# Performance work log

Hardware: AMD Instinct MI355X
Metric: run time of the kernel (lower is better)

Reference implementation:

```python
import jax, jax.numpy as jnp
import numpy as np

N_IN = 2_000_000
N_OUT = 250_000
C_IN = 32
C_OUT = 64
K_VOL = 8  # 2x2x2 kernel, stride 2
EPS = 1e-5


def setup_inputs() -> dict:
    key = jax.random.key(0)
    ks = jax.random.split(key, 6)
    return {
        "in_feats": jax.random.normal(ks[0], (N_IN, C_IN), dtype=jnp.float32),
        "offset_id": jax.random.randint(ks[1], (N_IN,), 0, K_VOL, dtype=jnp.int32),
        "out_idx": jax.random.randint(ks[2], (N_IN,), 0, N_OUT, dtype=jnp.int32),
        "weight": jax.random.normal(ks[3], (K_VOL, C_IN, C_OUT), dtype=jnp.float32) * 0.05,
        "gamma": jnp.ones((3, C_OUT), dtype=jnp.float32),
        "beta": jnp.zeros((3, C_OUT), dtype=jnp.float32),
        "context": jax.random.normal(ks[4], (256,), dtype=jnp.float32),
        "ctx_w": jax.random.normal(ks[5], (256, 2 * C_OUT), dtype=jnp.float32) * 0.02,
        "condition": 1,
    }


def reference(in_feats, offset_id, out_idx, weight, gamma, beta, context, ctx_w, condition):
    # --- sparse conv (stride == kernel): gather-GEMM-scatter per kernel tap ---
    out = jnp.zeros((N_OUT, C_OUT), dtype=in_feats.dtype)
    for k in range(K_VOL):  # fixed small loop over kernel taps
        xk = jnp.where((offset_id == k)[:, None], in_feats, 0.0)  # [N_in, C_in]
        contrib = xk @ weight[k]                                  # [N_in, C_out]
        out = out + jax.ops.segment_sum(contrib, out_idx, num_segments=N_OUT)
    # --- conditional BN (PDNorm-style): per-channel stats, condition-selected affine ---
    mean = jnp.mean(out, axis=0)
    var = jnp.var(out, axis=0)
    normed = (out - mean) * jax.lax.rsqrt(var + EPS)
    normed = normed * gamma[condition] + beta[condition]
    # context modulation: scale/shift from context vector
    scale, shift = jnp.split(context @ ctx_w, 2)  # each [C_out]
    normed = normed * (1.0 + scale) + shift
    # --- ReLU ---
    return jax.nn.relu(normed)
```

## Files before the change

### kernel.cpp

```cpp
#include <hip/hip_runtime.h>

#define N_IN 2000000
#define N_OUT 250000
#define C_IN 32
#define C_OUT 64
#define K_VOL 8
#define EPS 1e-5f
#define CAP 32

#define PT_BLOCKS 7813
#define N_SCAN 250112
#define N_SBLK 977

typedef __attribute__((ext_vector_type(8))) short short8;
typedef __attribute__((ext_vector_type(4))) float f32x4;

#define TA_WHL    250368
#define TA_BSUM   266752
#define TA_SMALL  267776
#define TA_CNT    268288
#define TA_TAPB   518400
#define TA_XG     1018400
#define TA_POS    (TA_XG + N_IN * 32)
#define TA_NEED_BYTES ((size_t)(TA_POS + N_IN) * 4)

#define T1_WT     250000
#define T1_SMALL  266384
#define T1_RLIST  266768
#define T1_NEED_BYTES ((size_t)(T1_RLIST + N_OUT * CAP) * 4)

__global__ __launch_bounds__(256) void k_wpack(const float* __restrict__ w,
                                               ushort* __restrict__ whl) {
    int e = blockIdx.x * 256 + threadIdx.x;
    int c = e >> 11, t = (e >> 9) & 3, l = (e >> 3) & 63, kp = e & 7;
    int j = 4 * c + (l >> 4);
    int n = t * 16 + (l & 15);
    float v = w[kp * 2048 + j * 64 + n];
    unsigned bits = __float_as_uint(v);
    float lo = v - __uint_as_float(bits & 0xFFFF0000u);
    whl[e]         = (ushort)(bits >> 16);
    whl[16384 + e] = (ushort)(__float_as_uint(lo) >> 16);
}


__global__ __launch_bounds__(256) void k_rank(const int* __restrict__ out_idx,
                                              int* __restrict__ cnt,
                                              int* __restrict__ pos0) {
    int i = blockIdx.x * 256 + threadIdx.x;
    if (i < N_IN) pos0[i] = atomicAdd(&cnt[out_idx[i]], 1);
}

__global__ __launch_bounds__(256) void k_scan_a(const int* __restrict__ cnt,
                                                int* __restrict__ S,
                                                int* __restrict__ bsum) {
    __shared__ int sh[256];
    int t = threadIdx.x;
    int g = blockIdx.x * 256 + t;
    int v = cnt[g];
    sh[t] = v;
    __syncthreads();
#pragma unroll
    for (int off = 1; off < 256; off <<= 1) {
        int a = (t >= off) ? sh[t - off] : 0;
        __syncthreads();
        sh[t] += a;
        __syncthreads();
    }
    S[g] = sh[t] - v;
    if (t == 255) bsum[blockIdx.x] = sh[255];
}

__global__ __launch_bounds__(1024) void k_scan_b(int* __restrict__ bsum) {
    __shared__ int sh[1024];
    int t = threadIdx.x;
    int v = (t < N_SBLK) ? bsum[t] : 0;
    sh[t] = v;
    __syncthreads();
#pragma unroll
    for (int off = 1; off < 1024; off <<= 1) {
        int a = (t >= off) ? sh[t - off] : 0;
        __syncthreads();
        sh[t] += a;
        __syncthreads();
    }
    bsum[t] = sh[t] - v;
}

__global__ __launch_bounds__(256) void k_scan_c(int* __restrict__ S,
                                                const int* __restrict__ bsum) {
    int g = blockIdx.x * 256 + threadIdx.x;
    S[g] += bsum[blockIdx.x];
}

__global__ __launch_bounds__(256) void k_scat3(const int* __restrict__ out_idx,
                                               const int* __restrict__ offs,
                                               const int* __restrict__ pos0,
                                               const int* __restrict__ S,
                                               const float* __restrict__ xf,
                                               float* __restrict__ xg,
                                               unsigned char* __restrict__ tb) {
    int lane = threadIdx.x & 63;
    int wid = (blockIdx.x * 256 + threadIdx.x) >> 6;
    int g = lane >> 3, e = lane & 7;
    const int STRIDE = PT_BLOCKS * 4 * 8;
    for (int p0 = wid * 8; p0 < N_IN; p0 += STRIDE) {
        int p = p0 + g;
        float4 x = *(const float4*)(xf + (size_t)p * 32 + e * 4);
        int pos = 0;
        if (e == 0) {
            int o = out_idx[p];
            pos = S[o] + pos0[p];
            tb[pos] = (unsigned char)(offs[p] | ((o & 31) << 3));
        }
        pos = __shfl(pos, g * 8, 64);
        *(float4*)(xg + (size_t)pos * 32 + e * 4) = x;
    }
}

__global__ __launch_bounds__(256) void k_gconv6(const float* __restrict__ xg,
                                                const unsigned char* __restrict__ tb,
                                                const int* __restrict__ Sarr,
                                                const ushort* __restrict__ whl,
                                                float* __restrict__ out) {
    __shared__ float vxl[4 * 4640];
    int lane = threadIdx.x & 63;
    int wv = threadIdx.x >> 6;
    int g = blockIdx.x * 4 + wv;
    int base = g * 16;
    if (base >= N_OUT) return;
    float* VX = vxl + wv * 4640;
    short* XT = (short*)VX;

    int s = Sarr[base];
    int e = Sarr[base + 16];
    int slot = lane >> 3, jq = lane & 7;

    int tgt8[8];
#pragma unroll
    for (int m = 0; m < 8; ++m) {
        int bin0 = m * 16 + (lane & 15);
        tgt8[m] = (((base + (bin0 >> 3)) & 31) << 3) | (bin0 & 7);
    }

    f32x4 acc1[8][2];
#pragma unroll
    for (int m = 0; m < 8; ++m)
#pragma unroll
        for (int n = 0; n < 2; ++n)
            acc1[m][n] = (f32x4){0.f, 0.f, 0.f, 0.f};

    auto LOADBLK = [&](int p0, float4* xvv, int* tvv) {
#pragma unroll
        for (int q = 0; q < 4; ++q) {
            int p = p0 + q * 8 + slot;
            int pc = p < e ? p : e - 1;
            xvv[q] = *(const float4*)(xg + (size_t)pc * 32 + jq * 4);
            tvv[q] = tb[pc];
            if (p >= e) xvv[q] = make_float4(0.f, 0.f, 0.f, 0.f);
        }
    };
    auto STAGE = [&](int bb, const float4* xvv, const int* tvv) {
        short* Xh = XT + bb * 3104;
        short* Xl = Xh + 1536;
        unsigned char* TGb = (unsigned char*)(Xh + 3072);
#pragma unroll
        for (int q = 0; q < 4; ++q) {
            int wpos = ((q ^ (jq & 3)) << 3) + slot;
#pragma unroll
            for (int i = 0; i < 4; ++i) {
                float v = (i == 0) ? xvv[q].x : (i == 1) ? xvv[q].y
                         : (i == 2) ? xvv[q].z : xvv[q].w;
                unsigned b = __float_as_uint(v);
                float lo = v - __uint_as_float(b & 0xFFFF0000u);
                int ch = 4 * jq + i;
                Xh[ch * 48 + wpos] = (short)(b >> 16);
                Xl[ch * 48 + wpos] = (short)(__float_as_uint(lo) >> 16);
            }
            if (jq == 0) TGb[q * 8 + slot] = (unsigned char)tvv[q];
        }
    };

    if (e > s) {
        float4 xv[4], xv2[4];
        int tv[4], tv2[4];
        LOADBLK(s, xv, tv);
        STAGE(0, xv, tv);
        int nIt = (e - s + 31) >> 5;
        for (int it = 0; it < nIt; ++it) {
            int cur = it & 1;
            bool more = (it + 1 < nIt);
            if (more) LOADBLK(s + (it + 1) * 32, xv2, tv2);

            asm volatile("s_waitcnt lgkmcnt(0)" ::: "memory");

            const short* Xh = XT + cur * 3104;
            const short* Xl = Xh + 1536;
            const unsigned char* TGb = (const unsigned char*)(Xh + 3072);
            unsigned long long t8 = *(const unsigned long long*)(TGb + 8 * (lane >> 4));
            int tgv[8];
#pragma unroll
            for (int e2 = 0; e2 < 8; ++e2) tgv[e2] = (int)((t8 >> (8 * e2)) & 0xFF);
            short8 bhf[2], blf[2];
#pragma unroll
            for (int n = 0; n < 2; ++n) {
                int ch = n * 16 + (lane & 15);
                int off = ch * 48 + 8 * ((lane >> 4) ^ ((ch >> 2) & 3));
                bhf[n] = *(const short8*)(Xh + off);
                blf[n] = *(const short8*)(Xl + off);
            }
#pragma unroll
            for (int m = 0; m < 8; ++m) {
                short8 ah;
#pragma unroll
                for (int e2 = 0; e2 < 8; ++e2)
                    ah[e2] = (tgv[e2] == tgt8[m]) ? (short)0x3F80 : (short)0;
#pragma unroll
                for (int n = 0; n < 2; ++n) {
                    acc1[m][n] = __builtin_amdgcn_mfma_f32_16x16x32_bf16(ah, bhf[n], acc1[m][n], 0, 0, 0);
                    acc1[m][n] = __builtin_amdgcn_mfma_f32_16x16x32_bf16(ah, blf[n], acc1[m][n], 0, 0, 0);
                }
            }

            if (more) {
                STAGE(cur ^ 1, xv2, tv2);
#pragma unroll
                for (int q = 0; q < 4; ++q) { xv[q] = xv2[q]; tv[q] = tv2[q]; }
            }
        }
    }

    asm volatile("s_waitcnt lgkmcnt(0)" ::: "memory");

#pragma unroll
    for (int m = 0; m < 8; ++m)
#pragma unroll
        for (int n = 0; n < 2; ++n)
#pragma unroll
            for (int reg = 0; reg < 4; ++reg) {
                int bin = m * 16 + (lane >> 4) * 4 + reg;
                VX[(bin >> 3) * 289 + (n * 16 + (lane & 15)) * 9 + (bin & 7)] = acc1[m][n][reg];
            }

    __builtin_amdgcn_sched_barrier(0);
    asm volatile("s_waitcnt lgkmcnt(0)" ::: "memory");
    __builtin_amdgcn_sched_barrier(0);

    int o = lane >> 4;
    int n16 = lane & 15;
    f32x4 zacc = {0.f, 0.f, 0.f, 0.f};
    f32x4 acc0 = zacc, accA = zacc, accB = zacc, accC = zacc;
    const short8* wh = (const short8*)whl;
    const short8* wl = wh + 2048;

#pragma unroll
    for (int c = 0; c < 8; ++c) {
        const float* src = VX + n16 * 289 + (4 * c + o) * 9;
        float a[8];
#pragma unroll
        for (int el = 0; el < 8; ++el) a[el] = src[el];
        short8 ahi, alo;
#pragma unroll
        for (int el = 0; el < 8; ++el) {
            unsigned b = __float_as_uint(a[el]);
            ahi[el] = (short)(b >> 16);
            float lo = a[el] - __uint_as_float(b & 0xFFFF0000u);
            alo[el] = (short)(__float_as_uint(lo) >> 16);
        }
#pragma unroll
        for (int t = 0; t < 4; ++t) {
            short8 bh = wh[(c * 4 + t) * 64 + lane];
            short8 bl = wl[(c * 4 + t) * 64 + lane];
            f32x4* pa = (t == 0) ? &acc0 : (t == 1) ? &accA : (t == 2) ? &accB : &accC;
            *pa = __builtin_amdgcn_mfma_f32_16x16x32_bf16(ahi, bh, *pa, 0, 0, 0);
            *pa = __builtin_amdgcn_mfma_f32_16x16x32_bf16(alo, bh, *pa, 0, 0, 0);
            *pa = __builtin_amdgcn_mfma_f32_16x16x32_bf16(ahi, bl, *pa, 0, 0, 0);
        }
    }

#pragma unroll
    for (int t = 0; t < 4; ++t) {
        f32x4 a = (t == 0) ? acc0 : (t == 1) ? accA : (t == 2) ? accB : accC;
#pragma unroll
        for (int reg = 0; reg < 4; ++reg)
            out[(size_t)(base + o * 4 + reg) * 64 + t * 16 + n16] = a[reg];
    }
}


__global__ __launch_bounds__(256) void k_stats(const float* __restrict__ out,
                                               float* __restrict__ sums,
                                               float* __restrict__ sumsq) {
    int t = threadIdx.x;
    long stride = (long)gridDim.x * 256;
    float s = 0.f, q = 0.f;
    for (long i = (long)blockIdx.x * 256 + t; i < (long)N_OUT * C_OUT; i += stride) {
        float v = out[i];
        s += v;
        q = fmaf(v, v, q);
    }
    __shared__ float ls[256], lq[256];
    ls[t] = s; lq[t] = q;
    __syncthreads();
    if (t < 64) {
        s = ls[t] + ls[t + 64] + ls[t + 128] + ls[t + 192];
        q = lq[t] + lq[t + 64] + lq[t + 128] + lq[t + 192];
        atomicAdd(&sums[t], s);
        atomicAdd(&sumsq[t], q);
    }
}

__global__ __launch_bounds__(256) void k_ctxprep(const float* __restrict__ context,
                                                 const float* __restrict__ ctx_w,
                                                 const float* __restrict__ sums,
                                                 const float* __restrict__ sumsq,
                                                 const float* __restrict__ gamma,
                                                 const float* __restrict__ beta,
                                                 const int* __restrict__ cond,
                                                 float* __restrict__ AB) {
    __shared__ float part[256];
    __shared__ float ctxv[128];
    int t = threadIdx.x;
    int col = t & 127, half = t >> 7;
    float s = 0.f;
    for (int r = half * 128; r < half * 128 + 128; ++r)
        s = fmaf(context[r], ctx_w[r * 128 + col], s);
    part[t] = s;
    __syncthreads();
    if (t < 128) ctxv[t] = part[t] + part[t + 128];
    __syncthreads();
    if (t < 64) {
        float mean = sums[t] * (1.f / N_OUT);
        float var  = sumsq[t] * (1.f / N_OUT) - mean * mean;
        float inv  = rsqrtf(var + EPS);
        int cd = cond[0];
        float gm = gamma[cd * C_OUT + t], bt = beta[cd * C_OUT + t];
        float sc = 1.f + ctxv[t];
        float sh = ctxv[64 + t];
        AB[t]      = inv * gm * sc;
        AB[64 + t] = (bt - mean * inv * gm) * sc + sh;
    }
}

__global__ __launch_bounds__(256) void k_norm(float* __restrict__ out,
                                              const float* __restrict__ AB) {
    __shared__ float4 lA[16], lB[16];
    int t = threadIdx.x;
    if (t < 16) {
        lA[t] = ((const float4*)AB)[t];
        lB[t] = ((const float4*)AB)[16 + t];
    }
    __syncthreads();
    const long total4 = (long)N_OUT * C_OUT / 4;
    long stride = (long)gridDim.x * 256;
    for (long i = (long)blockIdx.x * 256 + t; i < total4; i += stride) {
        float4 v = ((float4*)out)[i];
        float4 a = lA[i & 15], b = lB[i & 15];
        v.x = fmaxf(fmaf(v.x, a.x, b.x), 0.f);
        v.y = fmaxf(fmaf(v.y, a.y, b.y), 0.f);
        v.z = fmaxf(fmaf(v.z, a.z, b.z), 0.f);
        v.w = fmaxf(fmaf(v.w, a.w, b.w), 0.f);
        ((float4*)out)[i] = v;
    }
}


__global__ __launch_bounds__(256) void k_scat2(const int* __restrict__ out_idx,
                                               const int* __restrict__ offs,
                                               const float* __restrict__ w,
                                               int* __restrict__ cnt,
                                               int* __restrict__ rlist,
                                               ushort* __restrict__ whl) {
    int b = blockIdx.x;
    if (b < PT_BLOCKS) {
        int i = b * 256 + threadIdx.x;
        if (i < N_IN) {
            int o = out_idx[i];
            int pos = atomicAdd(&cnt[o], 1);
            if (pos < CAP) rlist[o * CAP + pos] = i | (offs[i] << 21);
        }
    } else {
        int e = (b - PT_BLOCKS) * 256 + threadIdx.x;
        int c = e >> 11, t = (e >> 9) & 3, l = (e >> 3) & 63, kp = e & 7;
        int j = 4 * c + (l >> 4);
        int n = t * 16 + (l & 15);
        float v = w[kp * 2048 + j * 64 + n];
        unsigned bits = __float_as_uint(v);
        float lo = v - __uint_as_float(bits & 0xFFFF0000u);
        whl[e]         = (ushort)(bits >> 16);
        whl[16384 + e] = (ushort)(__float_as_uint(lo) >> 16);
    }
}

__global__ __launch_bounds__(128) void k_gconv3(const float* __restrict__ xf,
                                                const int* __restrict__ cnt,
                                                const int* __restrict__ rlist,
                                                const ushort* __restrict__ whl,
                                                float* __restrict__ out) {
    __shared__ float vxl[2 * 4640];
    int lane = threadIdx.x & 63;
    int wv = threadIdx.x >> 6;
    int g = blockIdx.x * 2 + wv;
    int base = g * 16;
    if (base >= N_OUT) return;
    float* VX = vxl + wv * 4640;

    float4* z4 = (float4*)VX;
    float4 zz = make_float4(0.f, 0.f, 0.f, 0.f);
#pragma unroll
    for (int i = 0; i < 19; ++i) {
        int p = i * 64 + lane;
        if (p < 1156) z4[p] = zz;
    }

    int slot = lane >> 3, jq = lane & 7;
    int cv = cnt[base + (lane & 15)];
    const int* rbase = rlist + (size_t)base * CAP;
    int pkA = rbase[slot * CAP + jq];
    int pkB = rbase[(8 + slot) * CAP + jq];
    int pkC = rbase[slot * CAP + 8 + jq];
    int pkD = rbase[(8 + slot) * CAP + 8 + jq];

#pragma unroll
    for (int r = 0; r < 16; ++r) {
        int cr = __builtin_amdgcn_readlane(cv, r);
        if (cr > CAP) cr = CAP;
        if (cr == 0) continue;
        {
            int pk = __shfl(r < 8 ? pkA : pkB, (r & 7) * 8 + slot, 64);
            int idx = pk & 0x1FFFFF; if (idx > N_IN - 1) idx = N_IN - 1;
            int kp = (pk >> 21) & 7;
            const float4 x = *(const float4*)(xf + (size_t)idx * 32 + jq * 4);
            float* dst = VX + r * 289 + 36 * jq + kp;
            if (slot < cr) {
                atomicAdd(dst + 0,  x.x);
                atomicAdd(dst + 9,  x.y);
                atomicAdd(dst + 18, x.z);
                atomicAdd(dst + 27, x.w);
            }
        }
        if (cr > 8) {
            int pk = __shfl(r < 8 ? pkC : pkD, (r & 7) * 8 + slot, 64);
            int idx = pk & 0x1FFFFF; if (idx > N_IN - 1) idx = N_IN - 1;
            int kp = (pk >> 21) & 7;
            const float4 x = *(const float4*)(xf + (size_t)idx * 32 + jq * 4);
            float* dst = VX + r * 289 + 36 * jq + kp;
            if (8 + slot < cr) {
                atomicAdd(dst + 0,  x.x);
                atomicAdd(dst + 9,  x.y);
                atomicAdd(dst + 18, x.z);
                atomicAdd(dst + 27, x.w);
            }
        }
        if (cr > 16) {
            for (int p0 = 16; p0 < cr; p0 += 8) {
                int pp = p0 + slot; if (pp > cr - 1) pp = cr - 1;
                int pk = rlist[((size_t)base + r) * CAP + pp];
                int idx = pk & 0x1FFFFF; if (idx > N_IN - 1) idx = N_IN - 1;
                int kp = (pk >> 21) & 7;
                const float4 x = *(const float4*)(xf + (size_t)idx * 32 + jq * 4);
                float* dst = VX + r * 289 + 36 * jq + kp;
                if (p0 + slot < cr) {
                    atomicAdd(dst + 0,  x.x);
                    atomicAdd(dst + 9,  x.y);
                    atomicAdd(dst + 18, x.z);
                    atomicAdd(dst + 27, x.w);
                }
            }
        }
    }

    __builtin_amdgcn_sched_barrier(0);
    asm volatile("s_waitcnt lgkmcnt(0)" ::: "memory");
    __builtin_amdgcn_sched_barrier(0);

    int o = lane >> 4;
    int n16 = lane & 15;
    f32x4 zacc = {0.f, 0.f, 0.f, 0.f};
    f32x4 acc0 = zacc, acc1 = zacc, acc2 = zacc, acc3 = zacc;
    const short8* wh = (const short8*)whl;
    const short8* wl = wh + 2048;

#pragma unroll
    for (int c = 0; c < 8; ++c) {
        const float* src = VX + n16 * 289 + (4 * c + o) * 9;
        float a[8];
#pragma unroll
        for (int el = 0; el < 8; ++el) a[el] = src[el];
        short8 ahi, alo;
#pragma unroll
        for (int el = 0; el < 8; ++el) {
            unsigned b = __float_as_uint(a[el]);
            ahi[el] = (short)(b >> 16);
            float lo = a[el] - __uint_as_float(b & 0xFFFF0000u);
            alo[el] = (short)(__float_as_uint(lo) >> 16);
        }
#pragma unroll
        for (int t = 0; t < 4; ++t) {
            short8 bh = wh[(c * 4 + t) * 64 + lane];
            short8 bl = wl[(c * 4 + t) * 64 + lane];
            f32x4* pa = (t == 0) ? &acc0 : (t == 1) ? &acc1 : (t == 2) ? &acc2 : &acc3;
            *pa = __builtin_amdgcn_mfma_f32_16x16x32_bf16(ahi, bh, *pa, 0, 0, 0);
            *pa = __builtin_amdgcn_mfma_f32_16x16x32_bf16(alo, bh, *pa, 0, 0, 0);
            *pa = __builtin_amdgcn_mfma_f32_16x16x32_bf16(ahi, bl, *pa, 0, 0, 0);
        }
    }

#pragma unroll
    for (int t = 0; t < 4; ++t) {
        f32x4 a = (t == 0) ? acc0 : (t == 1) ? acc1 : (t == 2) ? acc2 : acc3;
#pragma unroll
        for (int reg = 0; reg < 4; ++reg)
            out[(size_t)(base + o * 4 + reg) * 64 + t * 16 + n16] = a[reg];
    }
}


extern "C" void kernel_launch(void* const* d_in, const int* in_sizes, int n_in,
                              void* d_out, int out_size, void* d_ws, size_t ws_size,
                              hipStream_t stream) {
    const float* in_feats = (const float*)d_in[0];
    const int*   offs     = (const int*)d_in[1];
    const int*   out_idx  = (const int*)d_in[2];
    const float* weight   = (const float*)d_in[3];
    const float* gamma    = (const float*)d_in[4];
    const float* beta     = (const float*)d_in[5];
    const float* context  = (const float*)d_in[6];
    const float* ctx_w    = (const float*)d_in[7];
    const int*   cond     = (const int*)d_in[8];
    float* out = (float*)d_out;

    int*   wsi = (int*)d_ws;
    float* wsf = (float*)d_ws;

    if (ws_size >= TA_NEED_BYTES) {
        int*    S      = wsi;
        ushort* whl    = (ushort*)(wsf + TA_WHL);
        int*    bsum   = wsi + TA_BSUM;
        float*  smalls = wsf + TA_SMALL;
        int*    cnt    = wsi + TA_CNT;
        unsigned char* tapb = (unsigned char*)(wsi + TA_TAPB);
        float*  xg     = wsf + TA_XG;
        int*    pos0   = wsi + TA_POS;

        hipMemsetAsync(cnt, 0, (size_t)N_SCAN * 4, stream);
        hipMemsetAsync(smalls, 0, 128 * 4, stream);

        k_rank<<<PT_BLOCKS, 256, 0, stream>>>(out_idx, cnt, pos0);
        k_scan_a<<<N_SBLK, 256, 0, stream>>>(cnt, S, bsum);
        k_scan_b<<<1, 1024, 0, stream>>>(bsum);
        k_scan_c<<<N_SBLK, 256, 0, stream>>>(S, bsum);
        k_wpack<<<64, 256, 0, stream>>>(weight, whl);
        k_scat3<<<PT_BLOCKS, 256, 0, stream>>>(out_idx, offs, pos0, S,
                                               in_feats, xg, tapb);
        k_gconv6<<<3907, 256, 0, stream>>>(xg, tapb, wsi, whl, out);

        k_stats<<<2048, 256, 0, stream>>>(out, smalls, smalls + 64);
        k_ctxprep<<<1, 256, 0, stream>>>(context, ctx_w, smalls, smalls + 64,
                                         gamma, beta, cond, smalls + 128);
        k_norm<<<2048, 256, 0, stream>>>(out, smalls + 128);
    } else {
        int*    cnt    = wsi;
        ushort* whl    = (ushort*)(wsf + T1_WT);
        float*  smalls = wsf + T1_SMALL;
        int*    rlist  = wsi + T1_RLIST;

        hipMemsetAsync(cnt, 0, (size_t)N_OUT * 4, stream);
        hipMemsetAsync(smalls, 0, 128 * 4, stream);

        k_scat2<<<PT_BLOCKS + 64, 256, 0, stream>>>(out_idx, offs, weight, cnt, rlist, whl);
        k_gconv3<<<7813, 128, 0, stream>>>(in_feats, cnt, rlist, whl, out);

        k_stats<<<2048, 256, 0, stream>>>(out, smalls, smalls + 64);
        k_ctxprep<<<1, 256, 0, stream>>>(context, ctx_w, smalls, smalls + 64,
                                         gamma, beta, cond, smalls + 128);
        k_norm<<<2048, 256, 0, stream>>>(out, smalls + 128);
    }
}
```

Before: 492.8 us.

## Scatter packed row indices instead of feature rows, gather features inside conv

The pre-pass no longer copies each 128-byte input feature row into a sorted buffer. It now writes one packed int per input point holding the original row index and the tap/output tag. The conv kernel reads these indices and gathers the feature rows directly from the original input. This removes a full write plus re-read of the feature array (about 256 MB each way). The cost is that the conv now does random gathers, and each feature load waits on a dependent index load.

```diff
diff --git a/kernel.cpp b/kernel.cpp
--- a/kernel.cpp
+++ b/kernel.cpp
@@ -19,9 +19,8 @@
 #define TA_BSUM   266752
 #define TA_SMALL  267776
 #define TA_CNT    268288
-#define TA_TAPB   518400
-#define TA_XG     1018400
-#define TA_POS    (TA_XG + N_IN * 32)
+#define TA_IDXG   1018400
+#define TA_POS    (TA_IDXG + N_IN)
 #define TA_NEED_BYTES ((size_t)(TA_POS + N_IN) * 4)
 
 #define T1_WT     250000
@@ -92,33 +91,20 @@
     S[g] += bsum[blockIdx.x];
 }
 
-__global__ __launch_bounds__(256) void k_scat3(const int* __restrict__ out_idx,
-                                               const int* __restrict__ offs,
-                                               const int* __restrict__ pos0,
-                                               const int* __restrict__ S,
-                                               const float* __restrict__ xf,
-                                               float* __restrict__ xg,
-                                               unsigned char* __restrict__ tb) {
-    int lane = threadIdx.x & 63;
-    int wid = (blockIdx.x * 256 + threadIdx.x) >> 6;
-    int g = lane >> 3, e = lane & 7;
-    const int STRIDE = PT_BLOCKS * 4 * 8;
-    for (int p0 = wid * 8; p0 < N_IN; p0 += STRIDE) {
-        int p = p0 + g;
-        float4 x = *(const float4*)(xf + (size_t)p * 32 + e * 4);
-        int pos = 0;
-        if (e == 0) {
-            int o = out_idx[p];
-            pos = S[o] + pos0[p];
-            tb[pos] = (unsigned char)(offs[p] | ((o & 31) << 3));
-        }
-        pos = __shfl(pos, g * 8, 64);
-        *(float4*)(xg + (size_t)pos * 32 + e * 4) = x;
-    }
-}
-
-__global__ __launch_bounds__(256) void k_gconv6(const float* __restrict__ xg,
-                                                const unsigned char* __restrict__ tb,
+__global__ __launch_bounds__(256) void k_scatidx(const int* __restrict__ out_idx,
+                                                 const int* __restrict__ offs,
+                                                 const int* __restrict__ pos0,
+                                                 const int* __restrict__ S,
+                                                 int* __restrict__ idxg) {
+    int i = blockIdx.x * 256 + threadIdx.x;
+    if (i >= N_IN) return;
+    int o = out_idx[i];
+    int tag = offs[i] | ((o & 31) << 3);
+    idxg[S[o] + pos0[i]] = i | (tag << 21);
+}
+
+__global__ __launch_bounds__(256) void k_gconv7(const float* __restrict__ xf,
+                                                const int* __restrict__ idxg,
                                                 const int* __restrict__ Sarr,
                                                 const ushort* __restrict__ whl,
                                                 float* __restrict__ out) {
@@ -150,12 +136,19 @@
             acc1[m][n] = (f32x4){0.f, 0.f, 0.f, 0.f};
 
     auto LOADBLK = [&](int p0, float4* xvv, int* tvv) {
+        int pk[4];
 #pragma unroll
         for (int q = 0; q < 4; ++q) {
             int p = p0 + q * 8 + slot;
             int pc = p < e ? p : e - 1;
-            xvv[q] = *(const float4*)(xg + (size_t)pc * 32 + jq * 4);
-            tvv[q] = tb[pc];
+            pk[q] = idxg[pc];
+        }
+#pragma unroll
+        for (int q = 0; q < 4; ++q) {
+            int p = p0 + q * 8 + slot;
+            int idx = pk[q] & 0x1FFFFF;
+            tvv[q] = (pk[q] >> 21) & 0xFF;
+            xvv[q] = *(const float4*)(xf + (size_t)idx * 32 + jq * 4);
             if (p >= e) xvv[q] = make_float4(0.f, 0.f, 0.f, 0.f);
         }
     };
@@ -538,8 +531,7 @@
         int*    bsum   = wsi + TA_BSUM;
         float*  smalls = wsf + TA_SMALL;
         int*    cnt    = wsi + TA_CNT;
-        unsigned char* tapb = (unsigned char*)(wsi + TA_TAPB);
-        float*  xg     = wsf + TA_XG;
+        int*    idxg   = wsi + TA_IDXG;
         int*    pos0   = wsi + TA_POS;
 
         hipMemsetAsync(cnt, 0, (size_t)N_SCAN * 4, stream);
@@ -550,9 +542,8 @@
         k_scan_b<<<1, 1024, 0, stream>>>(bsum);
         k_scan_c<<<N_SBLK, 256, 0, stream>>>(S, bsum);
         k_wpack<<<64, 256, 0, stream>>>(weight, whl);
-        k_scat3<<<PT_BLOCKS, 256, 0, stream>>>(out_idx, offs, pos0, S,
-                                               in_feats, xg, tapb);
-        k_gconv6<<<3907, 256, 0, stream>>>(xg, tapb, wsi, whl, out);
+        k_scatidx<<<PT_BLOCKS, 256, 0, stream>>>(out_idx, offs, pos0, S, idxg);
+        k_gconv7<<<3907, 256, 0, stream>>>(in_feats, idxg, wsi, whl, out);
 
         k_stats<<<2048, 256, 0, stream>>>(out, smalls, smalls + 64);
         k_ctxprep<<<1, 256, 0, stream>>>(context, ctx_w, smalls, smalls + 64,
```

Result: faster. 433.8 us (-12.0%).
